# Performance work log

Hardware: AMD Instinct MI355X
Metric: run time of the kernel (lower is better)

## Reference

```python
import jax, jax.numpy as jnp
import numpy as np

B = 65536            # batch of configurations
F = 32               # num_frames (joints)
DOF = 29             # controllable joints
# tree: chain 0..29, two mimic branches off frame 10; parent index always < child -> topo order = range(F)
PARENTS = [-1] + list(range(29)) + [10, 10]


def _np_rodrigues(w):
    th = np.linalg.norm(w)
    if th < 1e-12:
        return np.eye(3)
    k = w / th
    K = np.array([[0, -k[2], k[1]], [k[2], 0, -k[0]], [-k[1], k[0], 0]])
    return np.eye(3) + np.sin(th) * K + (1 - np.cos(th)) * (K @ K)


def setup_inputs() -> dict:
    key = jax.random.key(0)
    rng = np.random.default_rng(0)
    # joint types: 0 fixed, 1 revolute, 2 prismatic
    types = np.ones(F, dtype=np.int32)
    types[0] = 0
    types[15] = 2
    types[22] = 2
    # controllable = non-fixed, non-mimic (mimic dst = 30, 31)
    ctrl = np.array([i for i in range(F) if types[i] != 0 and i not in (30, 31)], dtype=np.int32)
    assert ctrl.shape[0] == DOF
    axes = rng.normal(size=(F, 3)).astype(np.float32)
    axes /= np.linalg.norm(axes, axis=-1, keepdims=True)
    origins = np.tile(np.eye(4, dtype=np.float32), (F, 1, 1))
    for i in range(F):
        origins[i, :3, :3] = _np_rodrigues(rng.normal(size=3) * 0.5)
        origins[i, :3, 3] = rng.normal(size=3) * 0.1
    joint_angles = jax.random.normal(key, (B, DOF), dtype=jnp.float32)
    return {
        "joint_angles": joint_angles,
        "all_axes": jnp.asarray(axes),
        "all_origins": jnp.asarray(origins),
        "mimic_multipliers": jnp.array([1.0, -1.0], dtype=jnp.float32),
        "mimic_offsets": jnp.array([0.1, -0.1], dtype=jnp.float32),
        "ctrlable_indices": jnp.asarray(ctrl),
        "mimic_src_indices": jnp.array([5, 6], dtype=jnp.int32),
        "mimic_dst_indices": jnp.array([30, 31], dtype=jnp.int32),
        "joint_types": jnp.asarray(types),
    }


def exp_map(w):
    # axis-angle (...,3) -> rotation (...,3,3), Rodrigues, eps-safe at w=0
    theta = jnp.sqrt(jnp.sum(w * w, axis=-1, keepdims=True) + 1e-18)  # (...,1)
    k = w / theta
    kx, ky, kz = k[..., 0], k[..., 1], k[..., 2]
    zero = jnp.zeros_like(kx)
    K = jnp.stack(
        [jnp.stack([zero, -kz, ky], -1),
         jnp.stack([kz, zero, -kx], -1),
         jnp.stack([-ky, kx, zero], -1)], -2)
    st = jnp.sin(theta)[..., None]
    ct = jnp.cos(theta)[..., None]
    return jnp.eye(3, dtype=w.dtype) + st * K + (1.0 - ct) * (K @ K)


def _fk(joint_angles, all_axes, all_origins, mimic_multipliers, mimic_offsets,
        ctrlable_indices, mimic_src_indices, mimic_dst_indices, joint_types):
    b = joint_angles.shape[0]
    # scatter controllable angles, then mimic gather/scatter
    all_angles = jnp.zeros((b, F), joint_angles.dtype).at[:, ctrlable_indices].set(joint_angles)
    mimic_vals = all_angles[:, mimic_src_indices] * mimic_multipliers + mimic_offsets
    all_angles = all_angles.at[:, mimic_dst_indices].set(mimic_vals)
    # per-frame local motion (B,F,4,4)
    w = all_axes[None, :, :] * all_angles[..., None]          # (B,F,3)
    R = exp_map(w)                                            # (B,F,3,3)
    R = jnp.where((joint_types == 1)[None, :, None, None], R, jnp.eye(3, dtype=w.dtype))
    t = jnp.where((joint_types == 2)[None, :, None], w, jnp.zeros((), w.dtype))
    top = jnp.concatenate([R, t[..., None]], axis=-1)         # (B,F,3,4)
    bottom = jnp.broadcast_to(jnp.array([0, 0, 0, 1], w.dtype), (b, F, 1, 4))
    motion = jnp.concatenate([top, bottom], axis=-2)          # (B,F,4,4)
    local = jnp.einsum('fij,bfjk->bfik', all_origins, motion)
    # sequential tree-structured compose (F is small & static -> unrolled)
    poses = []
    for i in range(F):
        p = PARENTS[i]
        li = local[:, i]
        poses.append(li if p < 0 else poses[p] @ li)
    return jnp.stack(poses, axis=1)                            # (B,F,4,4)


def reference(joint_angles, all_axes, all_origins, mimic_multipliers, mimic_offsets,
              ctrlable_indices, mimic_src_indices, mimic_dst_indices, joint_types):
    return _fk(joint_angles, all_axes, all_origins, mimic_multipliers, mimic_offsets,
               ctrlable_indices, mimic_src_indices, mimic_dst_indices, joint_types)
```

## Files before the change

### kernel.cpp

```cpp
#include <hip/hip_runtime.h>
#include <math.h>

#define NF 32
#define NDOF 29
#define BLOCK 256

__global__ __launch_bounds__(BLOCK) void fk_kernel(
    const float* __restrict__ ja,
    const float* __restrict__ axes,
    const float* __restrict__ origins,
    const float* __restrict__ mmul,
    const float* __restrict__ moff,
    const int*   __restrict__ ctrl,
    const int*   __restrict__ msrc,
    const int*   __restrict__ mdst,
    const int*   __restrict__ types,
    float*       __restrict__ out,
    int B)
{
    const int tid  = threadIdx.x;
    const int lane = tid & 63;
    const int f    = tid & 31;
    const long b   = (long)blockIdx.x * (BLOCK / 32) + (tid >> 5);
    if (b >= (long)B) return;

    int slot = -1;
    #pragma unroll
    for (int j = 0; j < NDOF; ++j) if (ctrl[j] == f) slot = j;
    float mu = 1.0f, of = 0.0f;
    #pragma unroll
    for (int m = 0; m < 2; ++m) {
        if (mdst[m] == f) {
            const int sf = msrc[m];
            #pragma unroll
            for (int j = 0; j < NDOF; ++j) if (ctrl[j] == sf) slot = j;
            mu = mmul[m]; of = moff[m];
        }
    }

    const float a  = (slot >= 0) ? fmaf(mu, ja[b * NDOF + slot], of) : 0.0f;
    const float wx = a * axes[f * 3 + 0];
    const float wy = a * axes[f * 3 + 1];
    const float wz = a * axes[f * 3 + 2];
    const int   ty = types[f];

    float R0,R1,R2,R3,R4,R5,R6,R7,R8;
    if (ty == 1) {
        const float t2 = wx*wx + wy*wy + wz*wz;
        const float th = sqrtf(t2 + 1e-18f);
        const float inv = 1.0f / th;
        const float kx = wx*inv, ky = wy*inv, kz = wz*inv;
        float s, c;
        __sincosf(th, &s, &c);
        const float v = 1.0f - c;
        R0 = fmaf(v*kx, kx, c);
        R1 = v*kx*ky - s*kz;
        R2 = v*kx*kz + s*ky;
        R3 = v*kx*ky + s*kz;
        R4 = fmaf(v*ky, ky, c);
        R5 = v*ky*kz - s*kx;
        R6 = v*kx*kz - s*ky;
        R7 = v*ky*kz + s*kx;
        R8 = fmaf(v*kz, kz, c);
    } else {
        R0=1.f;R1=0.f;R2=0.f;R3=0.f;R4=1.f;R5=0.f;R6=0.f;R7=0.f;R8=1.f;
    }
    const float tx  = (ty == 2) ? wx : 0.0f;
    const float tyv = (ty == 2) ? wy : 0.0f;
    const float tz  = (ty == 2) ? wz : 0.0f;

    float M[12];
    {
        const float4* O4 = (const float4*)origins;
        #pragma unroll
        for (int r = 0; r < 3; ++r) {
            const float4 O = O4[f * 4 + r];
            M[r*4+0] = O.x*R0 + O.y*R3 + O.z*R6;
            M[r*4+1] = O.x*R1 + O.y*R4 + O.z*R7;
            M[r*4+2] = O.x*R2 + O.y*R5 + O.z*R8;
            M[r*4+3] = O.x*tx + O.y*tyv + O.z*tz + O.w;
        }
    }

    int ptr = (f == 0) ? -1 : ((f >= 30) ? 10 : (f - 1));
    const int half = lane & 32;

    #pragma unroll
    for (int it = 0; it < 5; ++it) {
        const int src = half | (ptr & 31);
        float P[12];
        #pragma unroll
        for (int i = 0; i < 12; ++i) P[i] = __shfl(M[i], src, 64);
        const int pptr = __shfl(ptr, src, 64);
        if (ptr >= 0) {
            float N[12];
            #pragma unroll
            for (int r = 0; r < 3; ++r) {
                const float p0 = P[r*4+0], p1 = P[r*4+1], p2 = P[r*4+2], p3 = P[r*4+3];
                N[r*4+0] = p0*M[0] + p1*M[4] + p2*M[8];
                N[r*4+1] = p0*M[1] + p1*M[5] + p2*M[9];
                N[r*4+2] = p0*M[2] + p1*M[6] + p2*M[10];
                N[r*4+3] = p0*M[3] + p1*M[7] + p2*M[11] + p3;
            }
            #pragma unroll
            for (int i = 0; i < 12; ++i) M[i] = N[i];
            ptr = pptr;
        }
    }

    float4* o = (float4*)(out + b * 512 + f * 16);
    o[0] = make_float4(M[0], M[1], M[2],  M[3]);
    o[1] = make_float4(M[4], M[5], M[6],  M[7]);
    o[2] = make_float4(M[8], M[9], M[10], M[11]);
    o[3] = make_float4(0.0f, 0.0f, 0.0f,  1.0f);
}

extern "C" void kernel_launch(void* const* d_in, const int* in_sizes, int n_in,
                              void* d_out, int out_size, void* d_ws, size_t ws_size,
                              hipStream_t stream) {
    const float* ja   = (const float*)d_in[0];
    const float* axes = (const float*)d_in[1];
    const float* orig = (const float*)d_in[2];
    const float* mmul = (const float*)d_in[3];
    const float* moff = (const float*)d_in[4];
    const int*   ctrl = (const int*)d_in[5];
    const int*   msrc = (const int*)d_in[6];
    const int*   mdst = (const int*)d_in[7];
    const int*   typs = (const int*)d_in[8];
    float* out = (float*)d_out;

    const int B = in_sizes[0] / NDOF;
    const int batches_per_block = BLOCK / 32;
    const int grid = (B + batches_per_block - 1) / batches_per_block;
    fk_kernel<<<grid, BLOCK, 0, stream>>>(ja, axes, orig, mmul, moff,
                                          ctrl, msrc, mdst, typs, out, B);
}
```

Before: 180.2 us.

## Map 4 frames per thread with segmented prefix-scan compose and LDS-staged stores

Each thread now handles four consecutive frames, with eight lanes per configuration, so a block covers 32 configurations. The chain compose becomes a local sequential product followed by a three-step Hillis-Steele scan across the eight lanes, with the mimic branches fixed up from the frame-10 pose. Per-frame constants are staged in shared memory once per block, and outputs are transposed through shared memory so stores coalesce. This cuts shuffle rounds and redundant per-thread setup, at the cost of more registers (four 12-float matrices per thread) and extra LDS traffic.

Measured after the change: 163.6 us. 1.1x faster.

```diff
diff --git a/kernel.cpp b/kernel.cpp
--- a/kernel.cpp
+++ b/kernel.cpp
@@ -4,6 +4,20 @@
 #define NF 32
 #define NDOF 29
 #define BLOCK 256
+#define SLOT_DW 20
+
+__device__ __forceinline__ void amul(float* __restrict__ N,
+                                     const float* __restrict__ A,
+                                     const float* __restrict__ B) {
+    #pragma unroll
+    for (int r = 0; r < 3; ++r) {
+        const float a0 = A[r*4+0], a1 = A[r*4+1], a2 = A[r*4+2], a3 = A[r*4+3];
+        N[r*4+0] = a0*B[0] + a1*B[4] + a2*B[8];
+        N[r*4+1] = a0*B[1] + a1*B[5] + a2*B[9];
+        N[r*4+2] = a0*B[2] + a1*B[6] + a2*B[10];
+        N[r*4+3] = a0*B[3] + a1*B[7] + a2*B[11] + a3;
+    }
+}
 
 __global__ __launch_bounds__(BLOCK) void fk_kernel(
     const float* __restrict__ ja,
@@ -18,101 +32,179 @@
     float*       __restrict__ out,
     int B)
 {
+    __shared__ float s_ax[NF][3];
+    __shared__ float s_or[NF][12];
+    __shared__ int   s_type[NF];
+    __shared__ int   s_slot[NF];
+    __shared__ float s_mult[NF];
+    __shared__ float s_off[NF];
+    __shared__ float s_stage[4][64 * SLOT_DW];
+
     const int tid  = threadIdx.x;
     const int lane = tid & 63;
-    const int f    = tid & 31;
-    const long b   = (long)blockIdx.x * (BLOCK / 32) + (tid >> 5);
-    if (b >= (long)B) return;
-
-    int slot = -1;
-    #pragma unroll
-    for (int j = 0; j < NDOF; ++j) if (ctrl[j] == f) slot = j;
-    float mu = 1.0f, of = 0.0f;
-    #pragma unroll
-    for (int m = 0; m < 2; ++m) {
-        if (mdst[m] == f) {
-            const int sf = msrc[m];
+    const int wv   = tid >> 6;
+    const int sub  = lane & 7;
+    const int grp  = lane & ~7;
+
+    if (tid < NF) {
+        const int f = tid;
+        s_ax[f][0] = axes[f*3+0];
+        s_ax[f][1] = axes[f*3+1];
+        s_ax[f][2] = axes[f*3+2];
+        #pragma unroll
+        for (int i = 0; i < 12; ++i) s_or[f][i] = origins[f*16 + i];
+        s_type[f] = types[f];
+        int slot = -1;
+        for (int j = 0; j < NDOF; ++j) if (ctrl[j] == f) slot = j;
+        float mu = 1.0f, of = 0.0f;
+        for (int m = 0; m < 2; ++m) {
+            if (mdst[m] == f) {
+                const int sf = msrc[m];
+                for (int j = 0; j < NDOF; ++j) if (ctrl[j] == sf) slot = j;
+                mu = mmul[m]; of = moff[m];
+            }
+        }
+        s_slot[f] = slot; s_mult[f] = mu; s_off[f] = of;
+    }
+    __syncthreads();
+
+    const long bat = (long)blockIdx.x * 32 + (tid >> 3);
+    const bool bok = bat < (long)B;
+
+    float M[4][12];
+    #pragma unroll
+    for (int j = 0; j < 4; ++j) {
+        const int f    = 4*sub + j;
+        const int slot = s_slot[f];
+        float a = 0.0f;
+        if (slot >= 0 && bok) a = fmaf(s_mult[f], ja[bat * NDOF + slot], s_off[f]);
+        const float wx = a * s_ax[f][0];
+        const float wy = a * s_ax[f][1];
+        const float wz = a * s_ax[f][2];
+        const int ty = s_type[f];
+        float R0,R1,R2,R3,R4,R5,R6,R7,R8;
+        if (ty == 1) {
+            const float t2 = wx*wx + wy*wy + wz*wz;
+            const float th = sqrtf(t2 + 1e-18f);
+            const float inv = 1.0f / th;
+            const float kx = wx*inv, ky = wy*inv, kz = wz*inv;
+            float s, c;
+            __sincosf(th, &s, &c);
+            const float v = 1.0f - c;
+            R0 = fmaf(v*kx, kx, c);
+            R1 = v*kx*ky - s*kz;
+            R2 = v*kx*kz + s*ky;
+            R3 = v*kx*ky + s*kz;
+            R4 = fmaf(v*ky, ky, c);
+            R5 = v*ky*kz - s*kx;
+            R6 = v*kx*kz - s*ky;
+            R7 = v*ky*kz + s*kx;
+            R8 = fmaf(v*kz, kz, c);
+        } else {
+            R0=1.f;R1=0.f;R2=0.f;R3=0.f;R4=1.f;R5=0.f;R6=0.f;R7=0.f;R8=1.f;
+        }
+        const float tx  = (ty == 2) ? wx : 0.0f;
+        const float tyv = (ty == 2) ? wy : 0.0f;
+        const float tz  = (ty == 2) ? wz : 0.0f;
+        const float* O = s_or[f];
+        #pragma unroll
+        for (int r = 0; r < 3; ++r) {
+            const float o0 = O[r*4+0], o1 = O[r*4+1], o2 = O[r*4+2], o3 = O[r*4+3];
+            M[j][r*4+0] = o0*R0 + o1*R3 + o2*R6;
+            M[j][r*4+1] = o0*R1 + o1*R4 + o2*R7;
+            M[j][r*4+2] = o0*R2 + o1*R5 + o2*R8;
+            M[j][r*4+3] = o0*tx + o1*tyv + o2*tz + o3;
+        }
+    }
+
+    float I[12];
+    #pragma unroll
+    for (int i = 0; i < 12; ++i) I[i] = M[0][i];
+    #pragma unroll
+    for (int j = 1; j < 4; ++j) {
+        float N[12];
+        amul(N, I, M[j]);
+        const bool keep = !(sub == 7 && j >= 2);
+        #pragma unroll
+        for (int i = 0; i < 12; ++i) I[i] = keep ? N[i] : I[i];
+    }
+
+    #pragma unroll
+    for (int d = 1; d <= 4; d <<= 1) {
+        const int src = grp | ((sub - d) & 7);
+        float T[12];
+        #pragma unroll
+        for (int i = 0; i < 12; ++i) T[i] = __shfl(I[i], src, 64);
+        float N[12];
+        amul(N, T, I);
+        const bool use = (sub >= d);
+        #pragma unroll
+        for (int i = 0; i < 12; ++i) I[i] = use ? N[i] : I[i];
+    }
+
+    const float ID[12] = {1,0,0,0, 0,1,0,0, 0,0,1,0};
+    float run[12];
+    {
+        const int src = grp | ((sub - 1) & 7);
+        #pragma unroll
+        for (int i = 0; i < 12; ++i) {
+            const float t = __shfl(I[i], src, 64);
+            run[i] = (sub > 0) ? t : ID[i];
+        }
+    }
+
+    float P10[12];
+    #pragma unroll
+    for (int i = 0; i < 12; ++i) P10[i] = run[i];
+    #pragma unroll
+    for (int j = 0; j < 4; ++j) {
+        float N[12];
+        amul(N, run, M[j]);
+        const bool chain = !(sub == 7 && j >= 2);
+        #pragma unroll
+        for (int i = 0; i < 12; ++i) {
+            M[j][i] = chain ? N[i] : M[j][i];
+            run[i]  = chain ? N[i] : run[i];
+        }
+        if (j == 2 && sub == 2) {
             #pragma unroll
-            for (int j = 0; j < NDOF; ++j) if (ctrl[j] == sf) slot = j;
-            mu = mmul[m]; of = moff[m];
-        }
-    }
-
-    const float a  = (slot >= 0) ? fmaf(mu, ja[b * NDOF + slot], of) : 0.0f;
-    const float wx = a * axes[f * 3 + 0];
-    const float wy = a * axes[f * 3 + 1];
-    const float wz = a * axes[f * 3 + 2];
-    const int   ty = types[f];
-
-    float R0,R1,R2,R3,R4,R5,R6,R7,R8;
-    if (ty == 1) {
-        const float t2 = wx*wx + wy*wy + wz*wz;
-        const float th = sqrtf(t2 + 1e-18f);
-        const float inv = 1.0f / th;
-        const float kx = wx*inv, ky = wy*inv, kz = wz*inv;
-        float s, c;
-        __sincosf(th, &s, &c);
-        const float v = 1.0f - c;
-        R0 = fmaf(v*kx, kx, c);
-        R1 = v*kx*ky - s*kz;
-        R2 = v*kx*kz + s*ky;
-        R3 = v*kx*ky + s*kz;
-        R4 = fmaf(v*ky, ky, c);
-        R5 = v*ky*kz - s*kx;
-        R6 = v*kx*kz - s*ky;
-        R7 = v*ky*kz + s*kx;
-        R8 = fmaf(v*kz, kz, c);
-    } else {
-        R0=1.f;R1=0.f;R2=0.f;R3=0.f;R4=1.f;R5=0.f;R6=0.f;R7=0.f;R8=1.f;
-    }
-    const float tx  = (ty == 2) ? wx : 0.0f;
-    const float tyv = (ty == 2) ? wy : 0.0f;
-    const float tz  = (ty == 2) ? wz : 0.0f;
-
-    float M[12];
-    {
-        const float4* O4 = (const float4*)origins;
-        #pragma unroll
-        for (int r = 0; r < 3; ++r) {
-            const float4 O = O4[f * 4 + r];
-            M[r*4+0] = O.x*R0 + O.y*R3 + O.z*R6;
-            M[r*4+1] = O.x*R1 + O.y*R4 + O.z*R7;
-            M[r*4+2] = O.x*R2 + O.y*R5 + O.z*R8;
-            M[r*4+3] = O.x*tx + O.y*tyv + O.z*tz + O.w;
-        }
-    }
-
-    int ptr = (f == 0) ? -1 : ((f >= 30) ? 10 : (f - 1));
-    const int half = lane & 32;
-
-    #pragma unroll
-    for (int it = 0; it < 5; ++it) {
-        const int src = half | (ptr & 31);
-        float P[12];
-        #pragma unroll
-        for (int i = 0; i < 12; ++i) P[i] = __shfl(M[i], src, 64);
-        const int pptr = __shfl(ptr, src, 64);
-        if (ptr >= 0) {
-            float N[12];
-            #pragma unroll
-            for (int r = 0; r < 3; ++r) {
-                const float p0 = P[r*4+0], p1 = P[r*4+1], p2 = P[r*4+2], p3 = P[r*4+3];
-                N[r*4+0] = p0*M[0] + p1*M[4] + p2*M[8];
-                N[r*4+1] = p0*M[1] + p1*M[5] + p2*M[9];
-                N[r*4+2] = p0*M[2] + p1*M[6] + p2*M[10];
-                N[r*4+3] = p0*M[3] + p1*M[7] + p2*M[11] + p3;
-            }
-            #pragma unroll
-            for (int i = 0; i < 12; ++i) M[i] = N[i];
-            ptr = pptr;
-        }
-    }
-
-    float4* o = (float4*)(out + b * 512 + f * 16);
-    o[0] = make_float4(M[0], M[1], M[2],  M[3]);
-    o[1] = make_float4(M[4], M[5], M[6],  M[7]);
-    o[2] = make_float4(M[8], M[9], M[10], M[11]);
-    o[3] = make_float4(0.0f, 0.0f, 0.0f,  1.0f);
+            for (int i = 0; i < 12; ++i) P10[i] = N[i];
+        }
+    }
+    #pragma unroll
+    for (int i = 0; i < 12; ++i) P10[i] = __shfl(P10[i], grp | 2, 64);
+    #pragma unroll
+    for (int j = 2; j < 4; ++j) {
+        float N[12];
+        amul(N, P10, M[j]);
+        #pragma unroll
+        for (int i = 0; i < 12; ++i) M[j][i] = (sub == 7) ? N[i] : M[j][i];
+    }
+
+    float* const st = s_stage[wv];
+    const long wbat0 = (long)blockIdx.x * 32 + wv * 8;
+    float4* const out4 = (float4*)out;
+    const int row = lane & 3;
+
+    #pragma unroll
+    for (int j = 0; j < 4; ++j) {
+        float4* wp = (float4*)&st[lane * SLOT_DW];
+        wp[0] = make_float4(M[j][0], M[j][1], M[j][2],  M[j][3]);
+        wp[1] = make_float4(M[j][4], M[j][5], M[j][6],  M[j][7]);
+        wp[2] = make_float4(M[j][8], M[j][9], M[j][10], M[j][11]);
+        wp[3] = make_float4(0.0f, 0.0f, 0.0f, 1.0f);
+        __builtin_amdgcn_wave_barrier();
+        #pragma unroll
+        for (int m = 0; m < 4; ++m) {
+            const int  slot = m * 16 + (lane >> 2);
+            const float4 v  = *(const float4*)&st[slot * SLOT_DW + row * 4];
+            const long bb   = wbat0 + (slot >> 3);
+            const int  fr   = 4 * (slot & 7) + j;
+            if (bb < (long)B)
+                out4[bb * 128 + fr * 4 + row] = v;
+        }
+        __builtin_amdgcn_wave_barrier();
+    }
 }
 
 extern "C" void kernel_launch(void* const* d_in, const int* in_sizes, int n_in,
@@ -130,8 +222,7 @@
     float* out = (float*)d_out;
 
     const int B = in_sizes[0] / NDOF;
-    const int batches_per_block = BLOCK / 32;
-    const int grid = (B + batches_per_block - 1) / batches_per_block;
+    const int grid = (B + 31) / 32;
     fk_kernel<<<grid, BLOCK, 0, stream>>>(ja, axes, orig, mmul, moff,
                                           ctrl, msrc, mdst, typs, out, B);
 }
```
